# Optimization experiments

Hardware: AMD Instinct MI355X
Metric: run time of the kernel (lower is better)

The kernel has to match this reference:

```python
import jax, jax.numpy as jnp
import numpy as np

N_TOK, TOKDIM = 2048, 1024
NHEADS, KDIM = 16, 64


def setup_inputs() -> dict:
    key = jax.random.key(0)
    kg, kk, kq = jax.random.split(key, 3)
    g = jax.random.normal(kg, (N_TOK, TOKDIM), dtype=jnp.float32)
    # params use normal(stddev=0.002) init, as in the flax module
    Wk = 0.002 * jax.random.normal(kk, (NHEADS, KDIM, TOKDIM), dtype=jnp.float32)
    Wq = 0.002 * jax.random.normal(kq, (NHEADS, KDIM, TOKDIM), dtype=jnp.float32)
    return {"g": g, "Wk": Wk, "Wq": Wq}


def reference(g, Wk, Wq):
    """manual_grad of the attention energy: returns d(energy)/dg, shape [n, d]."""
    H, Z, D = Wk.shape
    betas = jnp.full((H,), 1.0, dtype=g.dtype) / jnp.sqrt(jnp.asarray(Z, g.dtype))
    K = jnp.einsum('hzd,kd->khz', Wk, g)   # [n,h,z]
    Q = jnp.einsum('hzd,qd->qhz', Wq, g)   # [n,h,z]
    F1 = jnp.einsum('hzd,khz->khd', Wq, K)  # [n,h,d]
    F2 = jnp.einsum('hzd,qhz->qhd', Wk, Q)  # [n,h,d]
    A1 = jnp.einsum('h,khz,qhz->hqk', betas, K, Q)  # [h,q,k] scores
    A2 = jax.nn.softmax(A1, -1)
    T1 = -jnp.einsum('khd,hqk->qd', F1, A2)
    T2 = -jnp.einsum('qhd,hqk->kd', F2, A2)
    return T1 + T2
```

## Files before the change

### kernel.cpp

```cpp
#include <hip/hip_runtime.h>
#include <stdint.h>

#define NT 2048
#define TD 1024
#define NH 16
static constexpr float SCL = 0.18033688011112042f;

typedef __attribute__((ext_vector_type(8))) short bf16x8;
typedef __attribute__((ext_vector_type(4))) float f32x4;
typedef __attribute__((ext_vector_type(16))) float f32x16;

__device__ __forceinline__ float bf2f(unsigned short u){
  union { uint32_t u32; float f; } v; v.u32 = ((uint32_t)u) << 16; return v.f;
}
__device__ __forceinline__ unsigned short f2bf(float f){
  union { float f; uint32_t u; } v; v.f = f;
  uint32_t r = v.u + 0x7fffu + ((v.u >> 16) & 1u);
  return (unsigned short)(r >> 16);
}

__global__ __launch_bounds__(256) void prep_kernel(
    const float* __restrict__ g, const float* __restrict__ Wk, const float* __restrict__ Wq,
    unsigned short* __restrict__ PG, unsigned short* __restrict__ PW,
    unsigned short* __restrict__ TWP)
{
  int b = blockIdx.x;
  int tid = threadIdx.x;
  if (b < 2048) {
    bool isW = (b >= 1024);
    int bb = isW ? b - 1024 : b;
    int dg = bb & 15, rb2 = bb >> 4;
    __shared__ float tile[32][65];
    const float* src;
    int rbase;
    if (!isW) { src = g; rbase = rb2 * 32; }
    else if (rb2 < 32) { src = Wk; rbase = rb2 * 32; }
    else { src = Wq; rbase = rb2 * 32 - 1024; }
    int r = tid >> 3, c0 = (tid & 7) * 8;
    const float* s = src + (size_t)(rbase + r) * 1024 + dg * 64 + c0;
    *(f32x4*)&tile[r][c0]     = *(const f32x4*)s;
    *(f32x4*)&tile[r][c0 + 4] = *(const f32x4*)(s + 4);
    __syncthreads();
    int dzl = tid >> 6, l = tid & 63;
    int dz = dg * 4 + dzl;
    unsigned short ob[8];
    #pragma unroll
    for (int e = 0; e < 8; e++)
      ob[e] = f2bf(tile[l & 31][dzl * 16 + 8 * (l >> 5) + e]);
    unsigned short* dst = (isW ? PW : PG) + ((size_t)(rb2 * 64 + dz) * 64 + l) * 8;
    *(ushort4*)dst       = *(ushort4*)&ob[0];
    *(ushort4*)(dst + 4) = *(ushort4*)&ob[4];
  } else {
    int t = b - 2048;
    int db = t & 31, jzg = t >> 5;
    int d0 = db * 32, j0 = jzg * 128;
    __shared__ unsigned short tile[128][33];
    const float* src = (j0 < 1024) ? Wq : Wk;
    int jb = (j0 < 1024) ? j0 : (j0 - 1024);
    #pragma unroll
    for (int i = 0; i < 16; i++) {
      int idx = i * 256 + tid, r = idx >> 5, c = idx & 31;
      tile[r][c] = f2bf(src[(size_t)(jb + r) * 1024 + d0 + c]);
    }
    __syncthreads();
    int jq = tid >> 6, l = tid & 63;
    #pragma unroll
    for (int f = 0; f < 2; f++) {
      int jzl = jq * 2 + f;
      unsigned short ob[8];
      #pragma unroll
      for (int e = 0; e < 8; e++)
        ob[e] = tile[jzl * 16 + 8 * (l >> 5) + e][l & 31];
      unsigned short* dst = TWP + ((size_t)(db * 128 + jzg * 8 + jzl) * 64 + l) * 8;
      *(ushort4*)dst       = *(ushort4*)&ob[0];
      *(ushort4*)(dst + 4) = *(ushort4*)&ob[4];
    }
  }
}

__global__ __launch_bounds__(256, 2) void kq_kernel(
    const unsigned short* __restrict__ PG,
    const unsigned short* __restrict__ PW,
    unsigned short* __restrict__ CKQ,
    unsigned short* __restrict__ PCK)
{
  __shared__ __align__(16) float Red[2][64][68];
  int tid = threadIdx.x, l = tid & 63, w = tid >> 6;
  int zr = l & 31, hi = l >> 5;
  int lin = blockIdx.x;
  int wgid = (lin & 7) * 128 + (lin >> 3);
  int tokb = wgid >> 5, cblk = wgid & 31;
  const bf16x8* PGf = (const bf16x8*)PG;
  const bf16x8* PWf = (const bf16x8*)PW;

  f32x16 acc[2][2] = {};
  bf16x8 a_c[2], b_c[2];
  auto loadx = [&](bf16x8 (&a_)[2], bf16x8 (&b_)[2], int dz){
    #pragma unroll
    for (int th = 0; th < 2; th++)
      a_[th] = PGf[((size_t)(tokb * 2 + th) * 64 + dz) * 64 + l];
    #pragma unroll
    for (int ch = 0; ch < 2; ch++)
      b_[ch] = PWf[((size_t)(cblk * 2 + ch) * 64 + dz) * 64 + l];
  };
  loadx(a_c, b_c, w * 16);
  for (int it = 0; it < 16; it++) {
    bf16x8 a_n[2], b_n[2];
    if (it + 1 < 16) loadx(a_n, b_n, w * 16 + it + 1);
    #pragma unroll
    for (int th = 0; th < 2; th++)
      #pragma unroll
      for (int ch = 0; ch < 2; ch++)
        acc[th][ch] = __builtin_amdgcn_mfma_f32_32x32x16_bf16(a_c[th], b_c[ch], acc[th][ch], 0, 0, 0);
    #pragma unroll
    for (int i = 0; i < 2; i++) { a_c[i] = a_n[i]; b_c[i] = b_n[i]; }
  }
  if (w >= 2) {
    #pragma unroll
    for (int th = 0; th < 2; th++)
      #pragma unroll
      for (int ch = 0; ch < 2; ch++) {
        int c = ch * 32 + zr;
        #pragma unroll
        for (int u = 0; u < 4; u++) {
          int tk = th * 32 + 8 * u + 4 * hi;
          f32x4 q;
          q[0] = acc[th][ch][4 * u];     q[1] = acc[th][ch][4 * u + 1];
          q[2] = acc[th][ch][4 * u + 2]; q[3] = acc[th][ch][4 * u + 3];
          *(f32x4*)&Red[w - 2][c][tk] = q;
        }
      }
  }
  __syncthreads();
  if (w < 2) {
    #pragma unroll
    for (int th = 0; th < 2; th++)
      #pragma unroll
      for (int ch = 0; ch < 2; ch++) {
        int c = ch * 32 + zr;
        #pragma unroll
        for (int u = 0; u < 4; u++) {
          int tk = th * 32 + 8 * u + 4 * hi;
          float* slot = &Red[w][c][tk];
          f32x4 q = *(f32x4*)slot;
          q[0] += acc[th][ch][4 * u];     q[1] += acc[th][ch][4 * u + 1];
          q[2] += acc[th][ch][4 * u + 2]; q[3] += acc[th][ch][4 * u + 3];
          *(f32x4*)slot = q;
        }
      }
  }
  __syncthreads();
  int p = tid >> 2, c16 = (tid & 3) * 16;
  int tok = tokb * 64 + p;
  unsigned short ob[16];
  #pragma unroll
  for (int i = 0; i < 16; i++)
    ob[i] = f2bf(Red[0][c16 + i][p] + Red[1][c16 + i][p]);
  unsigned short* dst = CKQ + (size_t)tok * 2048 + cblk * 64 + c16;
  *(ushort4*)dst        = *(ushort4*)&ob[0];
  *(ushort4*)(dst + 4)  = *(ushort4*)&ob[4];
  *(ushort4*)(dst + 8)  = *(ushort4*)&ob[8];
  *(ushort4*)(dst + 12) = *(ushort4*)&ob[12];
  int rb = tok >> 5, tl = tok & 31, kz = tid & 3;
  unsigned short* dstp = PCK + (((size_t)(cblk * 64 + rb) * 4 + kz) * 64) * 8;
  *(ushort4*)(dstp + tl * 8)            = *(ushort4*)&ob[0];
  *(ushort4*)(dstp + tl * 8 + 4)        = *(ushort4*)&ob[4];
  *(ushort4*)(dstp + (32 + tl) * 8)     = *(ushort4*)&ob[8];
  *(ushort4*)(dstp + (32 + tl) * 8 + 4) = *(ushort4*)&ob[12];
}

template<bool DIVL>
__global__ __launch_bounds__(256) void pack_pbx(const unsigned short* __restrict__ CKQ,
                                                const float* __restrict__ L,
                                                unsigned short* __restrict__ PBX)
{
  int bid = blockIdx.x;
  int qb = bid & 63, hz = bid >> 6;
  int h = hz >> 1, zb = hz & 1;
  int colbase = (DIVL ? 1024 : 0) + h * 64 + zb * 32;
  __shared__ unsigned short tq[32][36];
  __shared__ float rcpL[32];
  int tid = threadIdx.x;
  int r = tid >> 3, c0 = (tid & 7) * 4;
  *(ushort4*)&tq[r][c0] =
      *(const ushort4*)(CKQ + (size_t)(qb * 32 + r) * 2048 + colbase + c0);
  if (DIVL && tid < 32) rcpL[tid] = 1.0f / L[(size_t)h * NT + qb * 32 + tid];
  __syncthreads();
  if (tid < 128) {
    int ks = tid >> 6, l = tid & 63;
    int zl = l & 31, hi = l >> 5;
    unsigned short ob[8];
    #pragma unroll
    for (int e = 0; e < 8; e++) {
      int ql = 16 * ks + 8 * (e >> 2) + 4 * hi + (e & 3);
      unsigned short v = tq[ql][zl];
      if (DIVL) v = f2bf(bf2f(v) * rcpL[ql]);
      ob[e] = v;
    }
    unsigned short* dst = PBX + ((size_t)(bid * 2 + ks) * 64 + l) * 8;
    *(ushort4*)dst       = *(ushort4*)&ob[0];
    *(ushort4*)(dst + 4) = *(ushort4*)&ob[4];
  }
}

template<bool DIV>
__global__ __launch_bounds__(256, 2) void fused_kernel(
    const unsigned short* __restrict__ PCK,
    const unsigned short* __restrict__ PBX,
    unsigned short* __restrict__ PA,
    float* __restrict__ Lg)
{
  __shared__ __align__(16) float Red[2][64][68];
  __shared__ float L_lds[64];
  int tid = threadIdx.x, l = tid & 63, w = tid >> 6;
  int zr = l & 31, hi = l >> 5;
  int lin = blockIdx.x;
  int wgid = (lin & 7) * 64 + (lin >> 3);
  int h = wgid >> 5, pB = wgid & 31, p0 = pB * 64;
  int cbA = DIV ? h : 16 + h;
  int cbB = DIV ? 16 + h : h;
  const bf16x8* PCKf = (const bf16x8*)PCK;
  const bf16x8* PBXf = (const bf16x8*)PBX;

  bf16x8 bs[2][4];
  #pragma unroll
  for (int ps = 0; ps < 2; ps++)
    #pragma unroll
    for (int kz = 0; kz < 4; kz++)
      bs[ps][kz] = PCKf[((size_t)(cbB * 64 + pB * 2 + ps) * 4 + kz) * 64 + l];

  auto load = [&](bf16x8 (&a_)[4], bf16x8 (&pb_)[2][2], int rb){
    #pragma unroll
    for (int kz = 0; kz < 4; kz++)
      a_[kz] = PCKf[((size_t)(cbA * 64 + rb) * 4 + kz) * 64 + l];
    #pragma unroll
    for (int zb = 0; zb < 2; zb++)
      #pragma unroll
      for (int ks = 0; ks < 2; ks++)
        pb_[zb][ks] = PBXf[((size_t)((h * 2 + zb) * 64 + rb) * 2 + ks) * 64 + l];
  };

  f32x16 acc_pv[2][2] = {};
  float lsum[2] = {0.f, 0.f};
  bf16x8 a_c[4], pb_c[2][2];
  load(a_c, pb_c, w * 16);

  for (int t = 0; t < 16; t++) {
    bf16x8 a_n[4], pb_n[2][2];
    if (t + 1 < 16) load(a_n, pb_n, w * 16 + t + 1);
    f32x16 acc_s[2] = {};
    #pragma unroll
    for (int kz = 0; kz < 4; kz++) {
      acc_s[0] = __builtin_amdgcn_mfma_f32_32x32x16_bf16(a_c[kz], bs[0][kz], acc_s[0], 0, 0, 0);
      acc_s[1] = __builtin_amdgcn_mfma_f32_32x32x16_bf16(a_c[kz], bs[1][kz], acc_s[1], 0, 0, 0);
    }
    union { bf16x8 v; uint32_t u[4]; } pu[2][2];
    #pragma unroll
    for (int ps = 0; ps < 2; ps++) {
      float ev[16];
      #pragma unroll
      for (int r = 0; r < 16; r++) ev[r] = exp2f(acc_s[ps][r] * SCL);
      if (DIV) {
        #pragma unroll
        for (int r = 0; r < 16; r++) lsum[ps] += ev[r];
      }
      #pragma unroll
      for (int ks = 0; ks < 2; ks++)
        #pragma unroll
        for (int i = 0; i < 4; i++)
          asm("v_cvt_pk_bf16_f32 %0, %1, %2"
              : "=v"(pu[ps][ks].u[i]) : "v"(ev[8 * ks + 2 * i]), "v"(ev[8 * ks + 2 * i + 1]));
    }
    #pragma unroll
    for (int zb = 0; zb < 2; zb++)
      #pragma unroll
      for (int ks = 0; ks < 2; ks++) {
        acc_pv[0][zb] = __builtin_amdgcn_mfma_f32_32x32x16_bf16(pu[0][ks].v, pb_c[zb][ks], acc_pv[0][zb], 0, 0, 0);
        acc_pv[1][zb] = __builtin_amdgcn_mfma_f32_32x32x16_bf16(pu[1][ks].v, pb_c[zb][ks], acc_pv[1][zb], 0, 0, 0);
      }
    #pragma unroll
    for (int kz = 0; kz < 4; kz++) a_c[kz] = a_n[kz];
    #pragma unroll
    for (int zb = 0; zb < 2; zb++)
      #pragma unroll
      for (int ks = 0; ks < 2; ks++) pb_c[zb][ks] = pb_n[zb][ks];
  }

  if (w >= 2) {
    #pragma unroll
    for (int ps = 0; ps < 2; ps++)
      #pragma unroll
      for (int zb = 0; zb < 2; zb++) {
        int z = zb * 32 + zr;
        #pragma unroll
        for (int u = 0; u < 4; u++) {
          int p = ps * 32 + 8 * u + 4 * hi;
          f32x4 q;
          q[0] = acc_pv[ps][zb][4 * u];     q[1] = acc_pv[ps][zb][4 * u + 1];
          q[2] = acc_pv[ps][zb][4 * u + 2]; q[3] = acc_pv[ps][zb][4 * u + 3];
          *(f32x4*)&Red[w - 2][z][p] = q;
        }
      }
  }
  if (DIV && tid < 64) L_lds[tid] = 0.f;
  __syncthreads();
  if (w < 2) {
    #pragma unroll
    for (int ps = 0; ps < 2; ps++)
      #pragma unroll
      for (int zb = 0; zb < 2; zb++) {
        int z = zb * 32 + zr;
        #pragma unroll
        for (int u = 0; u < 4; u++) {
          int p = ps * 32 + 8 * u + 4 * hi;
          float* slot = &Red[w][z][p];
          f32x4 q = *(f32x4*)slot;
          q[0] += acc_pv[ps][zb][4 * u];     q[1] += acc_pv[ps][zb][4 * u + 1];
          q[2] += acc_pv[ps][zb][4 * u + 2]; q[3] += acc_pv[ps][zb][4 * u + 3];
          *(f32x4*)slot = q;
        }
      }
  }
  if (DIV) {
    #pragma unroll
    for (int ps = 0; ps < 2; ps++) {
      float s = lsum[ps];
      s += __shfl_xor(s, 32);
      if (hi == 0) atomicAdd(&L_lds[ps * 32 + zr], s);
    }
  }
  __syncthreads();
  if (DIV && tid < 64) Lg[(size_t)h * NT + p0 + tid] = L_lds[tid];
  int p = tid >> 2, z16 = (tid & 3) * 16;
  float inv = DIV ? 1.0f / L_lds[p] : 1.0f;
  int cbase = DIV ? h * 64 : TD + h * 64;
  int jz = (cbase + z16) >> 4;
  int tok = p0 + p, tb = tok >> 5, tl = tok & 31;
  unsigned short ob[16];
  #pragma unroll
  for (int i = 0; i < 16; i++) {
    int z = z16 + i;
    float x = Red[0][z][p] + Red[1][z][p];
    ob[i] = f2bf(x * inv);
  }
  unsigned short* dst = PA + (((size_t)jz * 64 + tb) * 64) * 8;
  *(ushort4*)(dst + tl * 8)            = *(ushort4*)&ob[0];
  *(ushort4*)(dst + tl * 8 + 4)        = *(ushort4*)&ob[4];
  *(ushort4*)(dst + (32 + tl) * 8)     = *(ushort4*)&ob[8];
  *(ushort4*)(dst + (32 + tl) * 8 + 4) = *(ushort4*)&ob[12];
}

__global__ __launch_bounds__(256, 2) void out_kernel(
    const unsigned short* __restrict__ PA,
    const unsigned short* __restrict__ TWP,
    float* __restrict__ out)
{
  __shared__ __align__(16) float Red[2][64][68];
  int tid = threadIdx.x, l = tid & 63, w = tid >> 6;
  int zr = l & 31, hi = l >> 5;
  int lin = blockIdx.x;
  int wgid = (lin & 7) * 64 + (lin >> 3);
  int tokb = wgid >> 4, db2 = wgid & 15;
  const bf16x8* PAf = (const bf16x8*)PA;
  const bf16x8* TWf = (const bf16x8*)TWP;

  f32x16 acc[2][2] = {};
  bf16x8 a_c[2], b_c[2];
  auto loadx = [&](bf16x8 (&a_)[2], bf16x8 (&b_)[2], int jz){
    #pragma unroll
    for (int th = 0; th < 2; th++)
      a_[th] = PAf[((size_t)jz * 64 + tokb * 2 + th) * 64 + l];
    #pragma unroll
    for (int dh = 0; dh < 2; dh++)
      b_[dh] = TWf[((size_t)(db2 * 2 + dh) * 128 + jz) * 64 + l];
  };
  loadx(a_c, b_c, w * 32);
  for (int it = 0; it < 32; it++) {
    bf16x8 a_n[2], b_n[2];
    if (it + 1 < 32) loadx(a_n, b_n, w * 32 + it + 1);
    #pragma unroll
    for (int th = 0; th < 2; th++)
      #pragma unroll
      for (int dh = 0; dh < 2; dh++)
        acc[th][dh] = __builtin_amdgcn_mfma_f32_32x32x16_bf16(a_c[th], b_c[dh], acc[th][dh], 0, 0, 0);
    #pragma unroll
    for (int i = 0; i < 2; i++) { a_c[i] = a_n[i]; b_c[i] = b_n[i]; }
  }
  if (w >= 2) {
    #pragma unroll
    for (int th = 0; th < 2; th++)
      #pragma unroll
      for (int dh = 0; dh < 2; dh++) {
        int d = dh * 32 + zr;
        #pragma unroll
        for (int u = 0; u < 4; u++) {
          int tk = th * 32 + 8 * u + 4 * hi;
          f32x4 q;
          q[0] = acc[th][dh][4 * u];     q[1] = acc[th][dh][4 * u + 1];
          q[2] = acc[th][dh][4 * u + 2]; q[3] = acc[th][dh][4 * u + 3];
          *(f32x4*)&Red[w - 2][d][tk] = q;
        }
      }
  }
  __syncthreads();
  if (w < 2) {
    #pragma unroll
    for (int th = 0; th < 2; th++)
      #pragma unroll
      for (int dh = 0; dh < 2; dh++) {
        int d = dh * 32 + zr;
        #pragma unroll
        for (int u = 0; u < 4; u++) {
          int tk = th * 32 + 8 * u + 4 * hi;
          float* slot = &Red[w][d][tk];
          f32x4 q = *(f32x4*)slot;
          q[0] += acc[th][dh][4 * u];     q[1] += acc[th][dh][4 * u + 1];
          q[2] += acc[th][dh][4 * u + 2]; q[3] += acc[th][dh][4 * u + 3];
          *(f32x4*)slot = q;
        }
      }
  }
  __syncthreads();
  int p = tid >> 2, d16 = (tid & 3) * 16;
  float* dst = out + (size_t)(tokb * 64 + p) * 1024 + db2 * 64 + d16;
  #pragma unroll
  for (int i4 = 0; i4 < 16; i4 += 4) {
    f32x4 r;
    #pragma unroll
    for (int j = 0; j < 4; j++)
      r[j] = -(Red[0][d16 + i4 + j][p] + Red[1][d16 + i4 + j][p]);
    *(f32x4*)(dst + i4) = r;
  }
}

extern "C" void kernel_launch(void* const* d_in, const int* in_sizes, int n_in,
                              void* d_out, int out_size, void* d_ws, size_t ws_size,
                              hipStream_t stream)
{
  (void)in_sizes; (void)n_in; (void)out_size; (void)ws_size;
  const float* g  = (const float*)d_in[0];
  const float* Wk = (const float*)d_in[1];
  const float* Wq = (const float*)d_in[2];

  char* ws = (char*)d_ws;
  size_t off = 0;
  auto alloc = [&](size_t b) -> char* {
    char* p = ws + off; off += (b + 255) & ~((size_t)255); return p;
  };
  unsigned short* PG   = (unsigned short*)alloc((size_t)NT * TD * 2);
  unsigned short* PW   = (unsigned short*)alloc((size_t)2048 * TD * 2);
  unsigned short* TWP  = (unsigned short*)alloc((size_t)TD * 2048 * 2);
  unsigned short* CKQ  = (unsigned short*)alloc((size_t)NT * 2048 * 2);
  unsigned short* PCK  = (unsigned short*)alloc((size_t)NT * 2048 * 2);
  unsigned short* PBT  = (unsigned short*)alloc((size_t)TD * NT * 2);
  unsigned short* QSTP = (unsigned short*)alloc((size_t)TD * NT * 2);
  unsigned short* PA   = (unsigned short*)alloc((size_t)NT * 2048 * 2);
  float*          Lbuf = (float*)alloc((size_t)NH * NT * 4);

  prep_kernel<<<dim3(2560), dim3(256), 0, stream>>>(g, Wk, Wq, PG, PW, TWP);

  kq_kernel<<<dim3(1024), dim3(256), 0, stream>>>(PG, PW, CKQ, PCK);

  pack_pbx<false><<<dim3(2048), dim3(256), 0, stream>>>(CKQ, nullptr, PBT);

  fused_kernel<true><<<dim3(512), dim3(256), 0, stream>>>(PCK, PBT, PA, Lbuf);

  pack_pbx<true><<<dim3(2048), dim3(256), 0, stream>>>(CKQ, Lbuf, QSTP);

  fused_kernel<false><<<dim3(512), dim3(256), 0, stream>>>(PCK, QSTP, PA, nullptr);

  out_kernel<<<dim3(512), dim3(256), 0, stream>>>(PA, TWP, (float*)d_out);
}
```

Before: 104.6 us.

## Fuse pbx packing into kq and fused kernels, drop CKQ and L buffers

Removes the two pack_pbx launches and the intermediate CKQ row-major buffer. kq_kernel now writes the transposed PBT layout straight from its LDS reduction tile. The first fused pass writes the L-normalised QSTP operand from its resident register tile through a new LDS transpose. This saves two launches and a round trip of the full key/query matrix through global memory. In exchange it adds LDS usage and extra epilogue work in kq_kernel and fused_kernel, which could affect occupancy.

```diff
diff --git a/kernel.cpp b/kernel.cpp
--- a/kernel.cpp
+++ b/kernel.cpp
@@ -81,8 +81,8 @@
 __global__ __launch_bounds__(256, 2) void kq_kernel(
     const unsigned short* __restrict__ PG,
     const unsigned short* __restrict__ PW,
-    unsigned short* __restrict__ CKQ,
-    unsigned short* __restrict__ PCK)
+    unsigned short* __restrict__ PCK,
+    unsigned short* __restrict__ PBT)
 {
   __shared__ __align__(16) float Red[2][64][68];
   int tid = threadIdx.x, l = tid & 63, w = tid >> 6;
@@ -156,50 +156,29 @@
   #pragma unroll
   for (int i = 0; i < 16; i++)
     ob[i] = f2bf(Red[0][c16 + i][p] + Red[1][c16 + i][p]);
-  unsigned short* dst = CKQ + (size_t)tok * 2048 + cblk * 64 + c16;
-  *(ushort4*)dst        = *(ushort4*)&ob[0];
-  *(ushort4*)(dst + 4)  = *(ushort4*)&ob[4];
-  *(ushort4*)(dst + 8)  = *(ushort4*)&ob[8];
-  *(ushort4*)(dst + 12) = *(ushort4*)&ob[12];
   int rb = tok >> 5, tl = tok & 31, kz = tid & 3;
   unsigned short* dstp = PCK + (((size_t)(cblk * 64 + rb) * 4 + kz) * 64) * 8;
   *(ushort4*)(dstp + tl * 8)            = *(ushort4*)&ob[0];
   *(ushort4*)(dstp + tl * 8 + 4)        = *(ushort4*)&ob[4];
   *(ushort4*)(dstp + (32 + tl) * 8)     = *(ushort4*)&ob[8];
   *(ushort4*)(dstp + (32 + tl) * 8 + 4) = *(ushort4*)&ob[12];
-}
-
-template<bool DIVL>
-__global__ __launch_bounds__(256) void pack_pbx(const unsigned short* __restrict__ CKQ,
-                                                const float* __restrict__ L,
-                                                unsigned short* __restrict__ PBX)
-{
-  int bid = blockIdx.x;
-  int qb = bid & 63, hz = bid >> 6;
-  int h = hz >> 1, zb = hz & 1;
-  int colbase = (DIVL ? 1024 : 0) + h * 64 + zb * 32;
-  __shared__ unsigned short tq[32][36];
-  __shared__ float rcpL[32];
-  int tid = threadIdx.x;
-  int r = tid >> 3, c0 = (tid & 7) * 4;
-  *(ushort4*)&tq[r][c0] =
-      *(const ushort4*)(CKQ + (size_t)(qb * 32 + r) * 2048 + colbase + c0);
-  if (DIVL && tid < 32) rcpL[tid] = 1.0f / L[(size_t)h * NT + qb * 32 + tid];
-  __syncthreads();
-  if (tid < 128) {
-    int ks = tid >> 6, l = tid & 63;
-    int zl = l & 31, hi = l >> 5;
-    unsigned short ob[8];
-    #pragma unroll
-    for (int e = 0; e < 8; e++) {
-      int ql = 16 * ks + 8 * (e >> 2) + 4 * hi + (e & 3);
-      unsigned short v = tq[ql][zl];
-      if (DIVL) v = f2bf(bf2f(v) * rcpL[ql]);
-      ob[e] = v;
-    }
-    unsigned short* dst = PBX + ((size_t)(bid * 2 + ks) * 64 + l) * 8;
-    *(ushort4*)dst       = *(ushort4*)&ob[0];
-    *(ushort4*)(dst + 4) = *(ushort4*)&ob[4];
+  if (cblk < 16) {
+    int h = cblk;
+    int zb = (tid >> 7) & 1, qh = (tid >> 6) & 1;
+    int cl = zb * 32 + zr;
+    #pragma unroll
+    for (int ks = 0; ks < 2; ks++) {
+      unsigned short o2[8];
+      #pragma unroll
+      for (int e = 0; e < 8; e++) {
+        int ql = 32 * qh + 16 * ks + 8 * (e >> 2) + 4 * hi + (e & 3);
+        o2[e] = f2bf(Red[0][cl][ql] + Red[1][cl][ql]);
+      }
+      unsigned short* dq = PBT +
+          ((((size_t)(h * 2 + zb) * 64 + tokb * 2 + qh) * 2 + ks) * 64 + l) * 8;
+      *(ushort4*)dq       = *(ushort4*)&o2[0];
+      *(ushort4*)(dq + 4) = *(ushort4*)&o2[4];
+    }
   }
 }
 
@@ -208,10 +187,11 @@
     const unsigned short* __restrict__ PCK,
     const unsigned short* __restrict__ PBX,
     unsigned short* __restrict__ PA,
-    float* __restrict__ Lg)
+    unsigned short* __restrict__ QSTP)
 {
   __shared__ __align__(16) float Red[2][64][68];
   __shared__ float L_lds[64];
+  __shared__ unsigned short Qt[64][68];
   int tid = threadIdx.x, l = tid & 63, w = tid >> 6;
   int zr = l & 31, hi = l >> 5;
   int lin = blockIdx.x;
@@ -330,7 +310,6 @@
     }
   }
   __syncthreads();
-  if (DIV && tid < 64) Lg[(size_t)h * NT + p0 + tid] = L_lds[tid];
   int p = tid >> 2, z16 = (tid & 3) * 16;
   float inv = DIV ? 1.0f / L_lds[p] : 1.0f;
   int cbase = DIV ? h * 64 : TD + h * 64;
@@ -348,6 +327,38 @@
   *(ushort4*)(dst + tl * 8 + 4)        = *(ushort4*)&ob[4];
   *(ushort4*)(dst + (32 + tl) * 8)     = *(ushort4*)&ob[8];
   *(ushort4*)(dst + (32 + tl) * 8 + 4) = *(ushort4*)&ob[12];
+
+  if (DIV) {
+    #pragma unroll
+    for (int ps = 0; ps < 2; ps++) {
+      float iq = 1.0f / L_lds[ps * 32 + zr];
+      #pragma unroll
+      for (int kz = 0; kz < 4; kz++) {
+        unsigned short t8[8];
+        #pragma unroll
+        for (int e = 0; e < 8; e++)
+          t8[e] = f2bf(bf2f((unsigned short)bs[ps][kz][e]) * iq);
+        unsigned short* qd = &Qt[ps * 32 + zr][kz * 16 + 8 * hi];
+        *(ushort4*)qd       = *(ushort4*)&t8[0];
+        *(ushort4*)(qd + 4) = *(ushort4*)&t8[4];
+      }
+    }
+    __syncthreads();
+    int zb = (tid >> 7) & 1, qh = (tid >> 6) & 1;
+    #pragma unroll
+    for (int ks = 0; ks < 2; ks++) {
+      unsigned short o2[8];
+      #pragma unroll
+      for (int e = 0; e < 8; e++) {
+        int ql = 32 * qh + 16 * ks + 8 * (e >> 2) + 4 * hi + (e & 3);
+        o2[e] = Qt[ql][zb * 32 + zr];
+      }
+      unsigned short* dq = QSTP +
+          ((((size_t)(h * 2 + zb) * 64 + pB * 2 + qh) * 2 + ks) * 64 + l) * 8;
+      *(ushort4*)dq       = *(ushort4*)&o2[0];
+      *(ushort4*)(dq + 4) = *(ushort4*)&o2[4];
+    }
+  }
 }
 
 __global__ __launch_bounds__(256, 2) void out_kernel(
@@ -450,22 +461,16 @@
   unsigned short* PG   = (unsigned short*)alloc((size_t)NT * TD * 2);
   unsigned short* PW   = (unsigned short*)alloc((size_t)2048 * TD * 2);
   unsigned short* TWP  = (unsigned short*)alloc((size_t)TD * 2048 * 2);
-  unsigned short* CKQ  = (unsigned short*)alloc((size_t)NT * 2048 * 2);
   unsigned short* PCK  = (unsigned short*)alloc((size_t)NT * 2048 * 2);
   unsigned short* PBT  = (unsigned short*)alloc((size_t)TD * NT * 2);
   unsigned short* QSTP = (unsigned short*)alloc((size_t)TD * NT * 2);
   unsigned short* PA   = (unsigned short*)alloc((size_t)NT * 2048 * 2);
-  float*          Lbuf = (float*)alloc((size_t)NH * NT * 4);
 
   prep_kernel<<<dim3(2560), dim3(256), 0, stream>>>(g, Wk, Wq, PG, PW, TWP);
 
-  kq_kernel<<<dim3(1024), dim3(256), 0, stream>>>(PG, PW, CKQ, PCK);
-
-  pack_pbx<false><<<dim3(2048), dim3(256), 0, stream>>>(CKQ, nullptr, PBT);
-
-  fused_kernel<true><<<dim3(512), dim3(256), 0, stream>>>(PCK, PBT, PA, Lbuf);
-
-  pack_pbx<true><<<dim3(2048), dim3(256), 0, stream>>>(CKQ, Lbuf, QSTP);
+  kq_kernel<<<dim3(1024), dim3(256), 0, stream>>>(PG, PW, PCK, PBT);
+
+  fused_kernel<true><<<dim3(512), dim3(256), 0, stream>>>(PCK, PBT, PA, QSTP);
 
   fused_kernel<false><<<dim3(512), dim3(256), 0, stream>>>(PCK, QSTP, PA, nullptr);
 
```

After: 99.01 us. 1.06x faster.
